# Optimization experiments

Hardware: AMD Instinct MI355X
Metric: run time of the kernel (lower is better)

Reference implementation:

```python
import jax, jax.numpy as jnp
import numpy as np

B, S, HID, HEADS = 1, 512, 1024, 16
HD = HID // HEADS          # 64
LN_EPS = 1e-5
EPS = 1e-8


def setup_inputs() -> dict:
    key = jax.random.key(0)
    ks = jax.random.split(key, 10)
    def w(k, fan_in, shape):
        return (jax.random.normal(k, shape, jnp.float32) / np.sqrt(fan_in)).astype(jnp.float32)
    return {
        "x": jax.random.normal(ks[0], (B, S, HID), jnp.float32),
        "attention_mask": jnp.ones((B, S), jnp.int32),
        "Wq": w(ks[1], HID, (HID, HID)), "bq": jnp.zeros((HID,), jnp.float32),
        "Wk": w(ks[2], HID, (HID, HID)), "bk": jnp.zeros((HID,), jnp.float32),
        "Wv": w(ks[3], HID, (HID, HID)), "bv": jnp.zeros((HID,), jnp.float32),
        "Wo": w(ks[4], HID, (HID, HID)), "bo": jnp.zeros((HID,), jnp.float32),
        "temperature": jnp.ones((1,), jnp.float32),
        "ln_gamma": jnp.ones((HID,), jnp.float32),
        "ln_beta": jnp.zeros((HID,), jnp.float32),
    }


def _forward(x, attention_mask, Wq, bq, Wk, bk, Wv, bv, Wo, bo, temperature, ln_gamma, ln_beta):
    b, s, hid = x.shape
    residual = x
    def proj(W, bias):  # [b,s,hid] -> [b,H,s,hd]
        return (x @ W + bias).reshape(b, s, HEADS, HD).transpose(0, 2, 1, 3)
    Q, K, V = proj(Wq, bq), proj(Wk, bk), proj(Wv, bv)
    # FFT over head_dim -> F = HD//2+1 frequency bins
    Qf = jnp.fft.rfft(Q, axis=-1)
    Kf = jnp.fft.rfft(K, axis=-1)
    Qa, Ka = jnp.abs(Qf), jnp.abs(Kf)
    Qp, Kp = jnp.angle(Qf), jnp.angle(Kf)
    # broadcast to [b,H,Sq,Sk,F]; eps lives inside sqrt (faithful, non-factorized)
    amp_w = jnp.sqrt(Qa[:, :, :, None, :] * Ka[:, :, None, :, :] + EPS)
    phase_align = jnp.cos(Qp[:, :, :, None, :] - Kp[:, :, None, :, :])
    scores = jnp.sum(phase_align * amp_w, axis=-1) * temperature  # [b,H,Sq,Sk]
    mask = attention_mask[:, None, None, :]  # [b,1,1,Sk]
    scores = jnp.where(mask == 0, jnp.float32(-1e9), scores)
    attn = jax.nn.softmax(scores, axis=-1)   # dropout omitted (eval mode)
    out = jnp.einsum('bhqk,bhkd->bhqd', attn, V)
    out = out.transpose(0, 2, 1, 3).reshape(b, s, hid)
    out = out @ Wo + bo
    y = residual + out
    mu = jnp.mean(y, axis=-1, keepdims=True)
    var = jnp.var(y, axis=-1, keepdims=True)
    return (y - mu) / jnp.sqrt(var + LN_EPS) * ln_gamma + ln_beta


def reference(x, attention_mask, Wq, bq, Wk, bk, Wv, bv, Wo, bo, temperature, ln_gamma, ln_beta):
    return _forward(x, attention_mask, Wq, bq, Wk, bk, Wv, bv, Wo, bo,
                    temperature, ln_gamma, ln_beta)
```

## Files before the change

kernel.cpp:

```cpp
#include <hip/hip_runtime.h>
#include <hip/hip_bf16.h>
#include <math.h>

constexpr int SEQ   = 512;
constexpr int HIDC  = 1024;
constexpr int NH    = 16;
constexpr int HDIM  = 64;
constexpr int NFREQ = 33;
constexpr int NFP   = 128;

typedef unsigned short u16;
typedef __bf16 bf16x8 __attribute__((ext_vector_type(8)));
typedef float  f32x4  __attribute__((ext_vector_type(4)));

typedef __attribute__((address_space(3))) void       as3_void;
typedef __attribute__((address_space(1))) const void as1_void;

__device__ __forceinline__ void gload16(const u16* g, u16* l) {
    __builtin_amdgcn_global_load_lds((as1_void*)g, (as3_void*)l, 16, 0, 0);
}

__device__ __forceinline__ float ldin(const void* p, int i, int f32) {
    if (f32) return ((const float*)p)[i];
    return __bfloat162float(((const __hip_bfloat16*)p)[i]);
}

__device__ __forceinline__ u16 f2b(float f) {
    unsigned int u = __builtin_bit_cast(unsigned int, f);
    u += 0x7fffu + ((u >> 16) & 1u);
    return (u16)(u >> 16);
}
__device__ __forceinline__ float b2f(u16 b) {
    return __builtin_bit_cast(float, (unsigned int)b << 16);
}
__device__ __forceinline__ void split2(float f, u16& hi, u16& lo) {
    hi = f2b(f);
    lo = f2b(f - b2f(hi));
}

__global__ void sniff_kernel(const void* w, int* flag) {
    __shared__ int cnt;
    if (threadIdx.x == 0) cnt = 0;
    __syncthreads();
    const unsigned short* h = (const unsigned short*)w;
    int bad = 0;
    for (int i = threadIdx.x; i < 512; i += 256) {
        const unsigned short v = h[i];
        const int ex = (v >> 7) & 0xFF;
        if (ex >= 134) bad++;
    }
    atomicAdd(&cnt, bad);
    __syncthreads();
    if (threadIdx.x == 0) flag[0] = (cnt > 32) ? 1 : 0;
}

__global__ __launch_bounds__(256) void prep_kernel(
    const void* __restrict__ W0, const void* __restrict__ W1,
    const void* __restrict__ W2, const void* __restrict__ W3,
    u16* __restrict__ H0, u16* __restrict__ L0,
    u16* __restrict__ H1, u16* __restrict__ L1,
    u16* __restrict__ H2, u16* __restrict__ L2,
    u16* __restrict__ H3, u16* __restrict__ L3,
    const void* __restrict__ xsrc, u16* __restrict__ xhi, u16* __restrict__ xlo,
    const int* __restrict__ flagp)
{
    const int F  = *flagp;
    const int mz = blockIdx.z;

    if (mz == 4) {
        const int blk = blockIdx.y * 16 + blockIdx.x;
        const int i0  = blk * 2048 + threadIdx.x * 8;
        #pragma unroll
        for (int g = 0; g < 2; ++g) {
            const int i = i0 + g * 4;
            float v[4];
            if (F) {
                const float4 f = *(const float4*)((const float*)xsrc + i);
                v[0] = f.x; v[1] = f.y; v[2] = f.z; v[3] = f.w;
            } else {
                #pragma unroll
                for (int j = 0; j < 4; ++j) v[j] = ldin(xsrc, i + j, 0);
            }
            ushort4 oh, ol;
            u16 h, l;
            split2(v[0], h, l); oh.x = h; ol.x = l;
            split2(v[1], h, l); oh.y = h; ol.y = l;
            split2(v[2], h, l); oh.z = h; ol.z = l;
            split2(v[3], h, l); oh.w = h; ol.w = l;
            *(ushort4*)&xhi[i] = oh;
            *(ushort4*)&xlo[i] = ol;
        }
        return;
    }

    __shared__ float t[64][65];
    const void* W = (mz == 0) ? W0 : (mz == 1) ? W1 : (mz == 2) ? W2 : W3;
    u16* H = (mz == 0) ? H0 : (mz == 1) ? H1 : (mz == 2) ? H2 : H3;
    u16* L = (mz == 0) ? L0 : (mz == 1) ? L1 : (mz == 2) ? L2 : L3;
    const int n0 = blockIdx.x * 64, k0 = blockIdx.y * 64;
    const int tid = threadIdx.x;

    #pragma unroll
    for (int i = 0; i < 4; ++i) {
        const int item = i * 256 + tid;
        const int r = item >> 4, c4 = (item & 15) * 4;
        if (F) {
            const float4 v = *(const float4*)((const float*)W + (k0 + r) * HIDC + n0 + c4);
            t[r][c4 + 0] = v.x; t[r][c4 + 1] = v.y; t[r][c4 + 2] = v.z; t[r][c4 + 3] = v.w;
        } else {
            #pragma unroll
            for (int j = 0; j < 4; ++j)
                t[r][c4 + j] = ldin(W, (k0 + r) * HIDC + n0 + c4 + j, 0);
        }
    }
    __syncthreads();
    #pragma unroll
    for (int i = 0; i < 4; ++i) {
        const int item = i * 256 + tid;
        const int r = item >> 4, c4 = (item & 15) * 4;
        ushort4 oh, ol;
        u16 h, l;
        split2(t[c4 + 0][r], h, l); oh.x = h; ol.x = l;
        split2(t[c4 + 1][r], h, l); oh.y = h; ol.y = l;
        split2(t[c4 + 2][r], h, l); oh.z = h; ol.z = l;
        split2(t[c4 + 3][r], h, l); oh.w = h; ol.w = l;
        *(ushort4*)&H[(n0 + r) * HIDC + k0 + c4] = oh;
        *(ushort4*)&L[(n0 + r) * HIDC + k0 + c4] = ol;
    }
}

template <int MODE>
__global__ __launch_bounds__(256) void mfma3_gemm_kernel(
    const u16* __restrict__ Ahi, const u16* __restrict__ Alo,
    const u16* __restrict__ B0h, const u16* __restrict__ B0l,
    const u16* __restrict__ B1h, const u16* __restrict__ B1l,
    const u16* __restrict__ B2h, const u16* __restrict__ B2l,
    const void* __restrict__ b0, const void* __restrict__ b1, const void* __restrict__ b2,
    const void* __restrict__ xres,
    float* __restrict__ O0, float* __restrict__ O1, float* __restrict__ O2,
    const int* __restrict__ flagp)
{
    __shared__ __align__(16) u16 smem[2 * 24576];
    const int F    = *flagp;
    const int tid  = threadIdx.x;
    const int lane = tid & 63, wv = tid >> 6;
    const int m0 = blockIdx.y * 64;
    const int n0 = blockIdx.x * 128;

    const u16 *Bh, *Bl; const void* bias; float* Out; int col0;
    if (MODE == 0) {
        const int mat = n0 >> 10;
        col0 = n0 & 1023;
        Bh   = (mat == 0) ? B0h : (mat == 1) ? B1h : B2h;
        Bl   = (mat == 0) ? B0l : (mat == 1) ? B1l : B2l;
        bias = (mat == 0) ? b0  : (mat == 1) ? b1  : b2;
        Out  = (mat == 0) ? O0  : (mat == 1) ? O1  : O2;
    } else {
        col0 = n0; Bh = B0h; Bl = B0l; bias = b0; Out = O0;
    }

    const int rsub = lane >> 3;
    const int gsw  = ((lane & 7) ^ rsub) * 8;
    const u16* pAh[2]; const u16* pAl[2];
    const u16* pBh[4]; const u16* pBl[4];
    int dA[2], dB[4];
    #pragma unroll
    for (int j = 0; j < 2; ++j) {
        const int c = wv * 2 + j;
        pAh[j] = Ahi + (m0 + c * 8 + rsub) * HIDC + gsw;
        pAl[j] = Alo + (m0 + c * 8 + rsub) * HIDC + gsw;
        dA[j]  = c * 512;
    }
    #pragma unroll
    for (int j = 0; j < 4; ++j) {
        const int c = wv * 4 + j;
        pBh[j] = Bh + (col0 + c * 8 + rsub) * HIDC + gsw;
        pBl[j] = Bl + (col0 + c * 8 + rsub) * HIDC + gsw;
        dB[j]  = c * 512;
    }

    int g16[2];
    #pragma unroll
    for (int kc = 0; kc < 2; ++kc) g16[kc] = (((kc * 4) + (lane >> 4)) ^ (lane & 7)) * 8;
    int afo[4], bfo[2];
    #pragma unroll
    for (int mi = 0; mi < 4; ++mi) afo[mi] = (mi * 16 + (lane & 15)) * 64;
    #pragma unroll
    for (int ni = 0; ni < 2; ++ni) bfo[ni] = (wv * 32 + ni * 16 + (lane & 15)) * 64;

    f32x4 zero = {0.f, 0.f, 0.f, 0.f};
    f32x4 acc[4][2];
    #pragma unroll
    for (int mi = 0; mi < 4; ++mi)
        #pragma unroll
        for (int ni = 0; ni < 2; ++ni) acc[mi][ni] = zero;

    #pragma unroll
    for (int j = 0; j < 2; ++j) {
        gload16(pAh[j], smem + dA[j]);
        gload16(pAl[j], smem + 4096 + dA[j]);
    }
    #pragma unroll
    for (int j = 0; j < 4; ++j) {
        gload16(pBh[j], smem + 8192  + dB[j]);
        gload16(pBl[j], smem + 16384 + dB[j]);
    }
    __syncthreads();

    for (int t = 0; t < 16; ++t) {
        const int bo = (t & 1) * 24576;
        if (t < 15) {
            const int bn = 24576 - bo;
            const int k  = (t + 1) * 64;
            #pragma unroll
            for (int j = 0; j < 2; ++j) {
                gload16(pAh[j] + k, smem + bn + dA[j]);
                gload16(pAl[j] + k, smem + bn + 4096 + dA[j]);
            }
            #pragma unroll
            for (int j = 0; j < 4; ++j) {
                gload16(pBh[j] + k, smem + bn + 8192  + dB[j]);
                gload16(pBl[j] + k, smem + bn + 16384 + dB[j]);
            }
        }
        #pragma unroll
        for (int kc = 0; kc < 2; ++kc) {
            bf16x8 ah[4], al[4], bh2[2], bl2[2];
            #pragma unroll
            for (int mi = 0; mi < 4; ++mi) {
                ah[mi] = *(const bf16x8*)(smem + bo +        afo[mi] + g16[kc]);
                al[mi] = *(const bf16x8*)(smem + bo + 4096 + afo[mi] + g16[kc]);
            }
            #pragma unroll
            for (int ni = 0; ni < 2; ++ni) {
                bh2[ni] = *(const bf16x8*)(smem + bo +  8192 + bfo[ni] + g16[kc]);
                bl2[ni] = *(const bf16x8*)(smem + bo + 16384 + bfo[ni] + g16[kc]);
            }
            #pragma unroll
            for (int mi = 0; mi < 4; ++mi)
                #pragma unroll
                for (int ni = 0; ni < 2; ++ni) {
                    acc[mi][ni] = __builtin_amdgcn_mfma_f32_16x16x32_bf16(
                        ah[mi], bh2[ni], acc[mi][ni], 0, 0, 0);
                    acc[mi][ni] = __builtin_amdgcn_mfma_f32_16x16x32_bf16(
                        ah[mi], bl2[ni], acc[mi][ni], 0, 0, 0);
                    acc[mi][ni] = __builtin_amdgcn_mfma_f32_16x16x32_bf16(
                        al[mi], bh2[ni], acc[mi][ni], 0, 0, 0);
                }
        }
        __syncthreads();
    }

    #pragma unroll
    for (int ni = 0; ni < 2; ++ni) {
        const int col = col0 + wv * 32 + ni * 16 + (lane & 15);
        const float bval = ldin(bias, col, F);
        #pragma unroll
        for (int mi = 0; mi < 4; ++mi) {
            const int row0 = m0 + mi * 16 + (lane >> 4) * 4;
            #pragma unroll
            for (int r = 0; r < 4; ++r) {
                const int row = row0 + r;
                float v = acc[mi][ni][r] + bval;
                if (MODE == 1) v += ldin(xres, row * HIDC + col, F);
                Out[row * HIDC + col] = v;
            }
        }
    }
}

__global__ __launch_bounds__(64) void spectral_kernel(
    const float* __restrict__ Q, const float* __restrict__ K,
    u16* __restrict__ Qsh, u16* __restrict__ Qsl,
    u16* __restrict__ Ksh, u16* __restrict__ Ksl)
{
    __shared__ float qv[64];
    __shared__ float tc[64], tsn[64];
    const int unit = blockIdx.x;
    const int sel  = blockIdx.y;
    const int s = unit >> 4, h = unit & 15;
    const float* src = sel ? K : Q;
    u16* dh = sel ? Ksh : Qsh;
    u16* dl = sel ? Ksl : Qsl;
    const int t = threadIdx.x;

    qv[t] = src[s * HIDC + h * HDIM + t];
    float sv, cv;
    sincosf((float)t * (6.283185307179586f / 64.0f), &sv, &cv);
    tc[t] = cv; tsn[t] = sv;
    __syncthreads();

    const int base = (h * SEQ + s) * NFP;
    if (t < NFREQ) {
        float re = 0.0f, im = 0.0f;
        #pragma unroll
        for (int k = 0; k < 64; ++k) {
            const int idx = (t * k) & 63;
            re = fmaf(qv[k], tc[idx], re);
            im = fmaf(qv[k], -tsn[idx], im);
        }
        const float a  = sqrtf(re * re + im * im);
        const float sc = (a > 0.0f) ? rsqrtf(a) : 0.0f;
        u16 hh, ll;
        split2(re * sc, hh, ll);
        dh[base + t] = hh; dl[base + t] = ll;
        split2(im * sc, hh, ll);
        dh[base + NFREQ + t] = hh; dl[base + NFREQ + t] = ll;
    }
    if (t < 62) {
        dh[base + 66 + t] = 0; dl[base + 66 + t] = 0;
    }
}

__global__ __launch_bounds__(256) void vtr_kernel(
    const float* __restrict__ V, u16* __restrict__ VTh, u16* __restrict__ VTl)
{
    __shared__ float t[64][65];
    const int s0 = blockIdx.x * 64, c0 = blockIdx.y * 64;
    const int tid = threadIdx.x;
    #pragma unroll
    for (int i = 0; i < 4; ++i) {
        const int item = i * 256 + tid;
        const int r = item >> 4, c4 = (item & 15) * 4;
        const float4 v = *(const float4*)&V[(s0 + r) * HIDC + c0 + c4];
        t[r][c4 + 0] = v.x; t[r][c4 + 1] = v.y; t[r][c4 + 2] = v.z; t[r][c4 + 3] = v.w;
    }
    __syncthreads();
    #pragma unroll
    for (int i = 0; i < 4; ++i) {
        const int item = i * 256 + tid;
        const int d = item >> 4, s4 = (item & 15) * 4;
        ushort4 oh, ol;
        u16 h, l;
        split2(t[s4 + 0][d], h, l); oh.x = h; ol.x = l;
        split2(t[s4 + 1][d], h, l); oh.y = h; ol.y = l;
        split2(t[s4 + 2][d], h, l); oh.z = h; ol.z = l;
        split2(t[s4 + 3][d], h, l); oh.w = h; ol.w = l;
        *(ushort4*)&VTh[(c0 + d) * SEQ + s0 + s4] = oh;
        *(ushort4*)&VTl[(c0 + d) * SEQ + s0 + s4] = ol;
    }
}

__global__ __launch_bounds__(128) void attn_mfma_kernel(
    const u16* __restrict__ Qsh, const u16* __restrict__ Qsl,
    const u16* __restrict__ Ksh, const u16* __restrict__ Ksl,
    const u16* __restrict__ VTh, const u16* __restrict__ VTl,
    const int* __restrict__ mask, const void* __restrict__ temp_p,
    u16* __restrict__ chi, u16* __restrict__ clo,
    const int* __restrict__ flagp)
{
    __shared__ __align__(16) u16 smem[32768];
    __shared__ int   mask_lds[512];
    __shared__ float mpart[2][16], lpart[2][16], l_final[16];

    const int F    = *flagp;
    const int tid  = threadIdx.x;
    const int lane = tid & 63, w = tid >> 6;
    const int hi = lane >> 4, q15 = lane & 15, l7 = lane & 7;
    const int h  = blockIdx.y, q0 = blockIdx.x * 16;
    const int k0 = w * 256;
    const int WB = w * 16384;
    const float temp = ldin(temp_p, 0, F);

    *(int4*)&mask_lds[tid * 4] = *(const int4*)&mask[tid * 4];

    bf16x8 qfh[3], qfl[3];
    {
        const int qrow = (h * SEQ + q0 + q15) * NFP;
        #pragma unroll
        for (int kc = 0; kc < 3; ++kc) {
            qfh[kc] = *(const bf16x8*)(Qsh + qrow + kc * 32 + hi * 8);
            qfl[kc] = *(const bf16x8*)(Qsl + qrow + kc * 32 + hi * 8);
        }
    }

    const int rc4 = lane >> 4;

    auto stageK = [&](int kt, int b) {
        const int base = WB + b * 8192;
        #pragma unroll
        for (int j = 0; j < 8; ++j) {
            const int row = j * 4 + rc4;
            const int gs  = (q15 ^ (row & 7)) * 8;
            const int so  = (h * SEQ + k0 + kt * 32 + row) * NFP + gs;
            gload16(Ksh + so, smem + base + j * 512);
            gload16(Ksl + so, smem + base + 4096 + j * 512);
        }
    };
    auto stageV = [&](int c, int b) {
        const int base = WB + b * 4096;
        #pragma unroll
        for (int j = 0; j < 4; ++j) {
            const int d  = j * 16 + (lane >> 2);
            const int gs = ((lane & 3) ^ (d & 3)) * 8;
            const int so = (h * HDIM + d) * SEQ + k0 + c * 32 + gs;
            gload16(VTh + so, smem + base + j * 512);
            gload16(VTl + so, smem + base + 2048 + j * 512);
        }
    };

    f32x4 sT[16];
    #pragma unroll
    for (int t = 0; t < 16; ++t) sT[t] = f32x4{0.f, 0.f, 0.f, 0.f};

    stageK(0, 0);
    #pragma unroll
    for (int kt = 0; kt < 8; ++kt) {
        if (kt < 7) {
            stageK(kt + 1, (kt + 1) & 1);
            asm volatile("s_waitcnt vmcnt(16)" ::: "memory");
        } else {
            asm volatile("s_waitcnt vmcnt(0)" ::: "memory");
        }
        __builtin_amdgcn_sched_barrier(0);
        const int base = WB + (kt & 1) * 8192;
        #pragma unroll
        for (int tt = 0; tt < 2; ++tt) {
            #pragma unroll
            for (int kc = 0; kc < 3; ++kc) {
                const int ro = (tt * 16 + q15) * 128 + (((kc * 4 + hi) ^ l7) * 8);
                const bf16x8 ah = *(const bf16x8*)(smem + base + ro);
                const bf16x8 al = *(const bf16x8*)(smem + base + 4096 + ro);
                sT[kt * 2 + tt] = __builtin_amdgcn_mfma_f32_16x16x32_bf16(ah, qfh[kc], sT[kt * 2 + tt], 0, 0, 0);
                sT[kt * 2 + tt] = __builtin_amdgcn_mfma_f32_16x16x32_bf16(ah, qfl[kc], sT[kt * 2 + tt], 0, 0, 0);
                sT[kt * 2 + tt] = __builtin_amdgcn_mfma_f32_16x16x32_bf16(al, qfh[kc], sT[kt * 2 + tt], 0, 0, 0);
            }
        }
    }

    __builtin_amdgcn_sched_barrier(0);
    stageV(0, 0);

    float m = -1e30f;
    #pragma unroll
    for (int t = 0; t < 16; ++t) {
        const int4 mv = *(const int4*)&mask_lds[k0 + t * 16 + hi * 4];
        float s;
        s = (mv.x == 0) ? -1e9f : sT[t][0] * temp; sT[t][0] = s; m = fmaxf(m, s);
        s = (mv.y == 0) ? -1e9f : sT[t][1] * temp; sT[t][1] = s; m = fmaxf(m, s);
        s = (mv.z == 0) ? -1e9f : sT[t][2] * temp; sT[t][2] = s; m = fmaxf(m, s);
        s = (mv.w == 0) ? -1e9f : sT[t][3] * temp; sT[t][3] = s; m = fmaxf(m, s);
    }
    m = fmaxf(m, __shfl_xor(m, 16, 64));
    m = fmaxf(m, __shfl_xor(m, 32, 64));
    if (lane < 16) mpart[w][q15] = m;
    __syncthreads();
    const float gm = fmaxf(mpart[0][q15], mpart[1][q15]);
    float sum = 0.0f;
    #pragma unroll
    for (int t = 0; t < 16; ++t) {
        #pragma unroll
        for (int r = 0; r < 4; ++r) {
            const float p = __expf(sT[t][r] - gm);
            sT[t][r] = p;
            sum += p;
        }
    }
    sum += __shfl_xor(sum, 16, 64);
    sum += __shfl_xor(sum, 32, 64);
    if (lane < 16) lpart[w][q15] = sum;
    __syncthreads();
    if (tid < 16) l_final[tid] = lpart[0][tid] + lpart[1][tid];

    const int PH = WB + 8192, PL = PH + 640;
    f32x4 acc[4];
    #pragma unroll
    for (int dt = 0; dt < 4; ++dt) acc[dt] = f32x4{0.f, 0.f, 0.f, 0.f};

    #pragma unroll
    for (int c = 0; c < 8; ++c) {
        if (c < 7) {
            stageV(c + 1, (c + 1) & 1);
            asm volatile("s_waitcnt vmcnt(8)" ::: "memory");
        } else {
            asm volatile("s_waitcnt vmcnt(0)" ::: "memory");
        }
        __builtin_amdgcn_sched_barrier(0);
        #pragma unroll
        for (int tt = 0; tt < 2; ++tt) {
            const int t = c * 2 + tt;
            ushort4 ph, pl;
            u16 hh, ll;
            split2(sT[t][0], hh, ll); ph.x = hh; pl.x = ll;
            split2(sT[t][1], hh, ll); ph.y = hh; pl.y = ll;
            split2(sT[t][2], hh, ll); ph.z = hh; pl.z = ll;
            split2(sT[t][3], hh, ll); ph.w = hh; pl.w = ll;
            const int g  = tt * 2 + (hi >> 1);
            const int po = q15 * 40 + ((g ^ (q15 & 3)) * 8) + (hi & 1) * 4;
            *(ushort4*)(smem + PH + po) = ph;
            *(ushort4*)(smem + PL + po) = pl;
        }
        const int vb  = WB + (c & 1) * 4096;
        const int pro = q15 * 40 + ((hi ^ (q15 & 3)) * 8);
        const bf16x8 pfh = *(const bf16x8*)(smem + PH + pro);
        const bf16x8 pfl = *(const bf16x8*)(smem + PL + pro);
        #pragma unroll
        for (int dt = 0; dt < 4; ++dt) {
            const int vo = (dt * 16 + q15) * 32 + ((hi ^ (q15 & 3)) * 8);
            const bf16x8 vfh = *(const bf16x8*)(smem + vb + vo);
            const bf16x8 vfl = *(const bf16x8*)(smem + vb + 2048 + vo);
            acc[dt] = __builtin_amdgcn_mfma_f32_16x16x32_bf16(pfh, vfh, acc[dt], 0, 0, 0);
            acc[dt] = __builtin_amdgcn_mfma_f32_16x16x32_bf16(pfl, vfh, acc[dt], 0, 0, 0);
            acc[dt] = __builtin_amdgcn_mfma_f32_16x16x32_bf16(pfh, vfl, acc[dt], 0, 0, 0);
        }
    }

    float* pacc = (float*)(smem + WB + 12288);
    #pragma unroll
    for (int dt = 0; dt < 4; ++dt)
        *(f32x4*)&pacc[(dt * 64 + lane) * 4] = acc[dt];
    __syncthreads();
    const float* pa0 = (const float*)(smem + 12288);
    const float* pa1 = (const float*)(smem + 16384 + 12288);
    #pragma unroll
    for (int dd = 0; dd < 2; ++dd) {
        const int dt = w * 2 + dd;
        #pragma unroll
        for (int r = 0; r < 4; ++r) {
            const int idx = (dt * 64 + lane) * 4 + r;
            const float v = (pa0[idx] + pa1[idx]) / l_final[hi * 4 + r];
            u16 hh, ll;
            split2(v, hh, ll);
            const int row = q0 + hi * 4 + r;
            const int col = h * HDIM + dt * 16 + q15;
            chi[row * HIDC + col] = hh;
            clo[row * HIDC + col] = ll;
        }
    }
}

__global__ __launch_bounds__(256) void ln_kernel(
    const float* __restrict__ Y, const void* __restrict__ gamma,
    const void* __restrict__ beta, void* __restrict__ out,
    const int* __restrict__ flagp)
{
    const int F = *flagp;
    const int row = blockIdx.x, tid = threadIdx.x;
    float v[4];
    float s = 0.0f, s2 = 0.0f;
    #pragma unroll
    for (int j = 0; j < 4; ++j) {
        v[j] = Y[row * HIDC + tid + j * 256];
        s += v[j]; s2 += v[j] * v[j];
    }
    #pragma unroll
    for (int off = 32; off > 0; off >>= 1) {
        s  += __shfl_xor(s, off, 64);
        s2 += __shfl_xor(s2, off, 64);
    }
    __shared__ float wred[4][2];
    const int w = tid >> 6;
    if ((tid & 63) == 0) { wred[w][0] = s; wred[w][1] = s2; }
    __syncthreads();
    s  = wred[0][0] + wred[1][0] + wred[2][0] + wred[3][0];
    s2 = wred[0][1] + wred[1][1] + wred[2][1] + wred[3][1];
    const float mu   = s / (float)HIDC;
    const float var  = s2 / (float)HIDC - mu * mu;
    const float rstd = rsqrtf(var + 1e-5f);
    #pragma unroll
    for (int j = 0; j < 4; ++j) {
        const int c = tid + j * 256;
        const float g = ldin(gamma, c, F), b = ldin(beta, c, F);
        const float r = (v[j] - mu) * rstd * g + b;
        if (F) ((float*)out)[row * HIDC + c] = r;
        else   ((__hip_bfloat16*)out)[row * HIDC + c] = __float2bfloat16(r);
    }
}

extern "C" void kernel_launch(void* const* d_in, const int* in_sizes, int n_in,
                              void* d_out, int out_size, void* d_ws, size_t ws_size,
                              hipStream_t stream) {
    const void* x    = d_in[0];
    const int*  mask = (const int*)d_in[1];
    const void* Wq   = d_in[2];
    const void* bq   = d_in[3];
    const void* Wk   = d_in[4];
    const void* bk   = d_in[5];
    const void* Wv   = d_in[6];
    const void* bv   = d_in[7];
    const void* Wo   = d_in[8];
    const void* bo   = d_in[9];
    const void* temp = d_in[10];
    const void* gam  = d_in[11];
    const void* bet  = d_in[12];

    float* ws   = (float*)d_ws;
    int*   flag = (int*)ws;
    float* Q    = ws + 4;
    float* K    = Q   + SEQ * HIDC;
    float* V    = K   + SEQ * HIDC;
    float* Y    = V   + SEQ * HIDC;
    u16*   xhi  = (u16*)(Y + SEQ * HIDC);
    u16*   xlo  = xhi + SEQ * HIDC;
    u16*   chi  = xlo + SEQ * HIDC;
    u16*   clo  = chi + SEQ * HIDC;
    u16*   Wqh  = clo + SEQ * HIDC;
    u16*   Wql  = Wqh + HIDC * HIDC;
    u16*   Wkh  = Wql + HIDC * HIDC;
    u16*   Wkl  = Wkh + HIDC * HIDC;
    u16*   Wvh  = Wkl + HIDC * HIDC;
    u16*   Wvl  = Wvh + HIDC * HIDC;
    u16*   Woh  = Wvl + HIDC * HIDC;
    u16*   Wol  = Woh + HIDC * HIDC;
    u16*   Qsh  = Wol + HIDC * HIDC;
    u16*   Qsl  = Qsh + NH * SEQ * NFP;
    u16*   Ksh  = Qsl + NH * SEQ * NFP;
    u16*   Ksl  = Ksh + NH * SEQ * NFP;
    u16*   VTh  = Ksl + NH * SEQ * NFP;
    u16*   VTl  = VTh + NH * HDIM * SEQ;

    sniff_kernel<<<1, 256, 0, stream>>>(Wq, flag);

    prep_kernel<<<dim3(16, 16, 5), 256, 0, stream>>>(
        Wq, Wk, Wv, Wo, Wqh, Wql, Wkh, Wkl, Wvh, Wvl, Woh, Wol,
        x, xhi, xlo, flag);

    mfma3_gemm_kernel<0><<<dim3(24, 8), 256, 0, stream>>>(
        xhi, xlo, Wqh, Wql, Wkh, Wkl, Wvh, Wvl,
        bq, bk, bv, nullptr, Q, K, V, flag);

    spectral_kernel<<<dim3(SEQ * NH, 2), 64, 0, stream>>>(Q, K, Qsh, Qsl, Ksh, Ksl);
    vtr_kernel<<<dim3(8, 16), 256, 0, stream>>>(V, VTh, VTl);

    attn_mfma_kernel<<<dim3(SEQ / 16, NH), 128, 0, stream>>>(
        Qsh, Qsl, Ksh, Ksl, VTh, VTl, mask, temp, chi, clo, flag);

    mfma3_gemm_kernel<1><<<dim3(8, 8), 256, 0, stream>>>(
        chi, clo, Woh, Wol, nullptr, nullptr, nullptr, nullptr,
        bo, nullptr, nullptr, x, Y, nullptr, nullptr, flag);

    ln_kernel<<<SEQ, 256, 0, stream>>>(Y, gam, bet, d_out, flag);
}
```

Baseline: 182.1 us.

## Fuse QKV epilogue into bf16 split, DFT via MFMA, inline dtype sniff

The QKV GEMM epilogue now writes hi/lo bf16 splits directly, and writes V already transposed, which removes the fp32 Q/K/V round trip and the separate transpose kernel. The per-token scalar spectral kernel becomes a batched DFT-as-GEMM kernel using MFMA against a cos/sin matrix built in registers. The standalone sniff kernel is removed and every kernel recomputes the dtype flag from a single wave read of Wq. The output projection moves to 32-row tiles so more blocks launch. This cuts launches and memory traffic, at the cost of redundant sniff loads and DFT rounding through split-bf16 MFMA.

New measurement: 161.6 us. 1.13x faster.

```diff
diff --git a/kernel.cpp b/kernel.cpp
--- a/kernel.cpp
+++ b/kernel.cpp
@@ -12,6 +12,7 @@
 typedef unsigned short u16;
 typedef __bf16 bf16x8 __attribute__((ext_vector_type(8)));
 typedef float  f32x4  __attribute__((ext_vector_type(4)));
+typedef unsigned short u16x8 __attribute__((ext_vector_type(8)));
 
 typedef __attribute__((address_space(3))) void       as3_void;
 typedef __attribute__((address_space(1))) const void as1_void;
@@ -38,20 +39,20 @@
     lo = f2b(f - b2f(hi));
 }
 
-__global__ void sniff_kernel(const void* w, int* flag) {
-    __shared__ int cnt;
-    if (threadIdx.x == 0) cnt = 0;
-    __syncthreads();
-    const unsigned short* h = (const unsigned short*)w;
+__device__ __forceinline__ int sniffF(const u16* wq) {
+    const int lane = threadIdx.x & 63;
+    const ushort4 a = *(const ushort4*)(wq + lane * 8);
+    const ushort4 b = *(const ushort4*)(wq + lane * 8 + 4);
     int bad = 0;
-    for (int i = threadIdx.x; i < 512; i += 256) {
-        const unsigned short v = h[i];
-        const int ex = (v >> 7) & 0xFF;
-        if (ex >= 134) bad++;
-    }
-    atomicAdd(&cnt, bad);
-    __syncthreads();
-    if (threadIdx.x == 0) flag[0] = (cnt > 32) ? 1 : 0;
+    {
+        const u16 vs[8] = {a.x, a.y, a.z, a.w, b.x, b.y, b.z, b.w};
+        #pragma unroll
+        for (int j = 0; j < 8; ++j)
+            if (((vs[j] >> 7) & 0xFF) >= 134) bad++;
+    }
+    #pragma unroll
+    for (int off = 32; off > 0; off >>= 1) bad += __shfl_xor(bad, off, 64);
+    return (bad > 32) ? 1 : 0;
 }
 
 __global__ __launch_bounds__(256) void prep_kernel(
@@ -61,10 +62,9 @@
     u16* __restrict__ H1, u16* __restrict__ L1,
     u16* __restrict__ H2, u16* __restrict__ L2,
     u16* __restrict__ H3, u16* __restrict__ L3,
-    const void* __restrict__ xsrc, u16* __restrict__ xhi, u16* __restrict__ xlo,
-    const int* __restrict__ flagp)
+    const void* __restrict__ xsrc, u16* __restrict__ xhi, u16* __restrict__ xlo)
 {
-    const int F  = *flagp;
+    const int F  = sniffF((const u16*)W0);
     const int mz = blockIdx.z;
 
     if (mz == 4) {
@@ -129,7 +129,7 @@
     }
 }
 
-template <int MODE>
+template <int MODE, int MT>
 __global__ __launch_bounds__(256) void mfma3_gemm_kernel(
     const u16* __restrict__ Ahi, const u16* __restrict__ Alo,
     const u16* __restrict__ B0h, const u16* __restrict__ B0l,
@@ -137,26 +137,33 @@
     const u16* __restrict__ B2h, const u16* __restrict__ B2l,
     const void* __restrict__ b0, const void* __restrict__ b1, const void* __restrict__ b2,
     const void* __restrict__ xres,
-    float* __restrict__ O0, float* __restrict__ O1, float* __restrict__ O2,
-    const int* __restrict__ flagp)
+    u16* __restrict__ Qh, u16* __restrict__ Ql,
+    u16* __restrict__ Kh, u16* __restrict__ Kl,
+    u16* __restrict__ Vth, u16* __restrict__ Vtl,
+    float* __restrict__ Yout,
+    const void* __restrict__ wq_sniff)
 {
-    __shared__ __align__(16) u16 smem[2 * 24576];
-    const int F    = *flagp;
+    constexpr int NMI = MT / 16;
+    constexpr int NAC = MT / 32;
+    constexpr int ACH = MT * 64;
+    constexpr int BUF = 2 * ACH + 16384;
+    __shared__ __align__(16) u16 smem[2 * BUF];
+
+    const int F    = sniffF((const u16*)wq_sniff);
     const int tid  = threadIdx.x;
     const int lane = tid & 63, wv = tid >> 6;
-    const int m0 = blockIdx.y * 64;
+    const int m0 = blockIdx.y * MT;
     const int n0 = blockIdx.x * 128;
 
-    const u16 *Bh, *Bl; const void* bias; float* Out; int col0;
+    const u16 *Bh, *Bl; const void* bias; int col0, mat = 0;
     if (MODE == 0) {
-        const int mat = n0 >> 10;
+        mat  = n0 >> 10;
         col0 = n0 & 1023;
         Bh   = (mat == 0) ? B0h : (mat == 1) ? B1h : B2h;
         Bl   = (mat == 0) ? B0l : (mat == 1) ? B1l : B2l;
         bias = (mat == 0) ? b0  : (mat == 1) ? b1  : b2;
-        Out  = (mat == 0) ? O0  : (mat == 1) ? O1  : O2;
     } else {
-        col0 = n0; Bh = B0h; Bl = B0l; bias = b0; Out = O0;
+        col0 = n0; Bh = B0h; Bl = B0l; bias = b0;
     }
 
     const int rsub = lane >> 3;
@@ -165,8 +172,8 @@
     const u16* pBh[4]; const u16* pBl[4];
     int dA[2], dB[4];
     #pragma unroll
-    for (int j = 0; j < 2; ++j) {
-        const int c = wv * 2 + j;
+    for (int j = 0; j < NAC; ++j) {
+        const int c = wv * NAC + j;
         pAh[j] = Ahi + (m0 + c * 8 + rsub) * HIDC + gsw;
         pAl[j] = Alo + (m0 + c * 8 + rsub) * HIDC + gsw;
         dA[j]  = c * 512;
@@ -184,60 +191,59 @@
     for (int kc = 0; kc < 2; ++kc) g16[kc] = (((kc * 4) + (lane >> 4)) ^ (lane & 7)) * 8;
     int afo[4], bfo[2];
     #pragma unroll
-    for (int mi = 0; mi < 4; ++mi) afo[mi] = (mi * 16 + (lane & 15)) * 64;
+    for (int mi = 0; mi < NMI; ++mi) afo[mi] = (mi * 16 + (lane & 15)) * 64;
     #pragma unroll
     for (int ni = 0; ni < 2; ++ni) bfo[ni] = (wv * 32 + ni * 16 + (lane & 15)) * 64;
 
-    f32x4 zero = {0.f, 0.f, 0.f, 0.f};
-    f32x4 acc[4][2];
-    #pragma unroll
-    for (int mi = 0; mi < 4; ++mi)
-        #pragma unroll
-        for (int ni = 0; ni < 2; ++ni) acc[mi][ni] = zero;
-
-    #pragma unroll
-    for (int j = 0; j < 2; ++j) {
+    f32x4 acc[NMI][2];
+    #pragma unroll
+    for (int mi = 0; mi < NMI; ++mi)
+        #pragma unroll
+        for (int ni = 0; ni < 2; ++ni) acc[mi][ni] = f32x4{0.f, 0.f, 0.f, 0.f};
+
+    #pragma unroll
+    for (int j = 0; j < NAC; ++j) {
         gload16(pAh[j], smem + dA[j]);
-        gload16(pAl[j], smem + 4096 + dA[j]);
+        gload16(pAl[j], smem + ACH + dA[j]);
     }
     #pragma unroll
     for (int j = 0; j < 4; ++j) {
-        gload16(pBh[j], smem + 8192  + dB[j]);
-        gload16(pBl[j], smem + 16384 + dB[j]);
+        gload16(pBh[j], smem + 2 * ACH + dB[j]);
+        gload16(pBl[j], smem + 2 * ACH + 8192 + dB[j]);
     }
     __syncthreads();
 
     for (int t = 0; t < 16; ++t) {
-        const int bo = (t & 1) * 24576;
+        const int bo = (t & 1) * BUF;
         if (t < 15) {
-            const int bn = 24576 - bo;
+            const int bn = BUF - bo;
             const int k  = (t + 1) * 64;
             #pragma unroll
-            for (int j = 0; j < 2; ++j) {
+            for (int j = 0; j < NAC; ++j) {
                 gload16(pAh[j] + k, smem + bn + dA[j]);
-                gload16(pAl[j] + k, smem + bn + 4096 + dA[j]);
+                gload16(pAl[j] + k, smem + bn + ACH + dA[j]);
             }
             #pragma unroll
             for (int j = 0; j < 4; ++j) {
-                gload16(pBh[j] + k, smem + bn + 8192  + dB[j]);
-                gload16(pBl[j] + k, smem + bn + 16384 + dB[j]);
+                gload16(pBh[j] + k, smem + bn + 2 * ACH + dB[j]);
+                gload16(pBl[j] + k, smem + bn + 2 * ACH + 8192 + dB[j]);
             }
         }
         #pragma unroll
         for (int kc = 0; kc < 2; ++kc) {
-            bf16x8 ah[4], al[4], bh2[2], bl2[2];
-            #pragma unroll
-            for (int mi = 0; mi < 4; ++mi) {
-                ah[mi] = *(const bf16x8*)(smem + bo +        afo[mi] + g16[kc]);
-                al[mi] = *(const bf16x8*)(smem + bo + 4096 + afo[mi] + g16[kc]);
+            bf16x8 ah[NMI], al[NMI], bh2[2], bl2[2];
+            #pragma unroll
+            for (int mi = 0; mi < NMI; ++mi) {
+                ah[mi] = *(const bf16x8*)(smem + bo +       afo[mi] + g16[kc]);
+                al[mi] = *(const bf16x8*)(smem + bo + ACH + afo[mi] + g16[kc]);
             }
             #pragma unroll
             for (int ni = 0; ni < 2; ++ni) {
-                bh2[ni] = *(const bf16x8*)(smem + bo +  8192 + bfo[ni] + g16[kc]);
-                bl2[ni] = *(const bf16x8*)(smem + bo + 16384 + bfo[ni] + g16[kc]);
-            }
-            #pragma unroll
-            for (int mi = 0; mi < 4; ++mi)
+                bh2[ni] = *(const bf16x8*)(smem + bo + 2 * ACH +        bfo[ni] + g16[kc]);
+                bl2[ni] = *(const bf16x8*)(smem + bo + 2 * ACH + 8192 + bfo[ni] + g16[kc]);
+            }
+            #pragma unroll
+            for (int mi = 0; mi < NMI; ++mi)
                 #pragma unroll
                 for (int ni = 0; ni < 2; ++ni) {
                     acc[mi][ni] = __builtin_amdgcn_mfma_f32_16x16x32_bf16(
@@ -251,93 +257,167 @@
         __syncthreads();
     }
 
+    const int hi4 = (lane >> 4) * 4;
     #pragma unroll
     for (int ni = 0; ni < 2; ++ni) {
         const int col = col0 + wv * 32 + ni * 16 + (lane & 15);
         const float bval = ldin(bias, col, F);
         #pragma unroll
-        for (int mi = 0; mi < 4; ++mi) {
-            const int row0 = m0 + mi * 16 + (lane >> 4) * 4;
-            #pragma unroll
-            for (int r = 0; r < 4; ++r) {
-                const int row = row0 + r;
-                float v = acc[mi][ni][r] + bval;
-                if (MODE == 1) v += ldin(xres, row * HIDC + col, F);
-                Out[row * HIDC + col] = v;
-            }
-        }
-    }
-}
-
-__global__ __launch_bounds__(64) void spectral_kernel(
-    const float* __restrict__ Q, const float* __restrict__ K,
+        for (int mi = 0; mi < NMI; ++mi) {
+            const int row0 = m0 + mi * 16 + hi4;
+            if (MODE == 1) {
+                #pragma unroll
+                for (int r = 0; r < 4; ++r) {
+                    const int row = row0 + r;
+                    Yout[row * HIDC + col] =
+                        acc[mi][ni][r] + bval + ldin(xres, row * HIDC + col, F);
+                }
+            } else if (mat == 2) {
+                ushort4 oh, ol;
+                u16 h_, l_;
+                split2(acc[mi][ni][0] + bval, h_, l_); oh.x = h_; ol.x = l_;
+                split2(acc[mi][ni][1] + bval, h_, l_); oh.y = h_; ol.y = l_;
+                split2(acc[mi][ni][2] + bval, h_, l_); oh.z = h_; ol.z = l_;
+                split2(acc[mi][ni][3] + bval, h_, l_); oh.w = h_; ol.w = l_;
+                *(ushort4*)&Vth[col * SEQ + row0] = oh;
+                *(ushort4*)&Vtl[col * SEQ + row0] = ol;
+            } else {
+                u16* Oh = (mat == 0) ? Qh : Kh;
+                u16* Ol = (mat == 0) ? Ql : Kl;
+                #pragma unroll
+                for (int r = 0; r < 4; ++r) {
+                    u16 h_, l_;
+                    split2(acc[mi][ni][r] + bval, h_, l_);
+                    Oh[(row0 + r) * HIDC + col] = h_;
+                    Ol[(row0 + r) * HIDC + col] = l_;
+                }
+            }
+        }
+    }
+}
+
+__global__ __launch_bounds__(256) void dft_kernel(
+    const u16* __restrict__ Qmh, const u16* __restrict__ Qml,
+    const u16* __restrict__ Kmh, const u16* __restrict__ Kml,
     u16* __restrict__ Qsh, u16* __restrict__ Qsl,
     u16* __restrict__ Ksh, u16* __restrict__ Ksl)
 {
-    __shared__ float qv[64];
-    __shared__ float tc[64], tsn[64];
-    const int unit = blockIdx.x;
-    const int sel  = blockIdx.y;
-    const int s = unit >> 4, h = unit & 15;
-    const float* src = sel ? K : Q;
-    u16* dh = sel ? Ksh : Qsh;
-    u16* dl = sel ? Ksl : Qsl;
-    const int t = threadIdx.x;
-
-    qv[t] = src[s * HIDC + h * HDIM + t];
-    float sv, cv;
-    sincosf((float)t * (6.283185307179586f / 64.0f), &sv, &cv);
-    tc[t] = cv; tsn[t] = sv;
-    __syncthreads();
-
-    const int base = (h * SEQ + s) * NFP;
-    if (t < NFREQ) {
-        float re = 0.0f, im = 0.0f;
-        #pragma unroll
-        for (int k = 0; k < 64; ++k) {
-            const int idx = (t * k) & 63;
-            re = fmaf(qv[k], tc[idx], re);
-            im = fmaf(qv[k], -tsn[idx], im);
-        }
-        const float a  = sqrtf(re * re + im * im);
-        const float sc = (a > 0.0f) ? rsqrtf(a) : 0.0f;
-        u16 hh, ll;
-        split2(re * sc, hh, ll);
-        dh[base + t] = hh; dl[base + t] = ll;
-        split2(im * sc, hh, ll);
-        dh[base + NFREQ + t] = hh; dl[base + NFREQ + t] = ll;
-    }
-    if (t < 62) {
-        dh[base + 66 + t] = 0; dl[base + 66 + t] = 0;
-    }
-}
-
-__global__ __launch_bounds__(256) void vtr_kernel(
-    const float* __restrict__ V, u16* __restrict__ VTh, u16* __restrict__ VTl)
-{
-    __shared__ float t[64][65];
-    const int s0 = blockIdx.x * 64, c0 = blockIdx.y * 64;
-    const int tid = threadIdx.x;
-    #pragma unroll
-    for (int i = 0; i < 4; ++i) {
-        const int item = i * 256 + tid;
-        const int r = item >> 4, c4 = (item & 15) * 4;
-        const float4 v = *(const float4*)&V[(s0 + r) * HIDC + c0 + c4];
-        t[r][c4 + 0] = v.x; t[r][c4 + 1] = v.y; t[r][c4 + 2] = v.z; t[r][c4 + 3] = v.w;
-    }
-    __syncthreads();
-    #pragma unroll
-    for (int i = 0; i < 4; ++i) {
-        const int item = i * 256 + tid;
-        const int d = item >> 4, s4 = (item & 15) * 4;
+    __shared__ __align__(16) u16 smem[16384];
+    __shared__ float tcos[64], tsin[64];
+
+    const int tid  = threadIdx.x;
+    const int lane = tid & 63, wv = tid >> 6;
+    const int hi = lane >> 4, q15 = lane & 15, l7 = lane & 7;
+    const int m0  = blockIdx.x * 64;
+    const int sel = blockIdx.y;
+    const u16* Ah_g = sel ? Kmh : Qmh;
+    const u16* Al_g = sel ? Kml : Qml;
+    u16* Oh = sel ? Ksh : Qsh;
+    u16* Ol = sel ? Ksl : Qsl;
+
+    const int rsub = lane >> 3;
+    const int gsw  = ((lane & 7) ^ rsub) * 8;
+    #pragma unroll
+    for (int j = 0; j < 2; ++j) {
+        const int c = wv * 2 + j;
+        gload16(Ah_g + (m0 + c * 8 + rsub) * 64 + gsw, smem + c * 512);
+        gload16(Al_g + (m0 + c * 8 + rsub) * 64 + gsw, smem + 4096 + c * 512);
+    }
+    if (tid < 64) {
+        float sv, cv;
+        sincosf((float)tid * (6.283185307179586f / 64.0f), &sv, &cv);
+        tcos[tid] = cv; tsin[tid] = sv;
+    }
+    __syncthreads();
+
+    bf16x8 Dh[2][2], Dl[2][2];
+    #pragma unroll
+    for (int ni = 0; ni < 2; ++ni) {
+        const int c = wv * 32 + ni * 16 + q15;
+        #pragma unroll
+        for (int kc = 0; kc < 2; ++kc) {
+            u16x8 bh_, bl_;
+            #pragma unroll
+            for (int e = 0; e < 8; ++e) {
+                const int k = (kc * 4 + hi) * 8 + e;
+                float dv;
+                if (c < 33)      dv = tcos[(c * k) & 63];
+                else if (c < 66) dv = -tsin[((c - 33) * k) & 63];
+                else             dv = 0.0f;
+                u16 h_, l_;
+                split2(dv, h_, l_);
+                bh_[e] = h_; bl_[e] = l_;
+            }
+            Dh[ni][kc] = __builtin_bit_cast(bf16x8, bh_);
+            Dl[ni][kc] = __builtin_bit_cast(bf16x8, bl_);
+        }
+    }
+
+    f32x4 acc[4][2];
+    #pragma unroll
+    for (int mi = 0; mi < 4; ++mi)
+        #pragma unroll
+        for (int ni = 0; ni < 2; ++ni) acc[mi][ni] = f32x4{0.f, 0.f, 0.f, 0.f};
+
+    #pragma unroll
+    for (int kc = 0; kc < 2; ++kc) {
+        const int g = (((kc * 4) + hi) ^ l7) * 8;
+        bf16x8 ah[4], al[4];
+        #pragma unroll
+        for (int mi = 0; mi < 4; ++mi) {
+            ah[mi] = *(const bf16x8*)(smem +        (mi * 16 + q15) * 64 + g);
+            al[mi] = *(const bf16x8*)(smem + 4096 + (mi * 16 + q15) * 64 + g);
+        }
+        #pragma unroll
+        for (int mi = 0; mi < 4; ++mi)
+            #pragma unroll
+            for (int ni = 0; ni < 2; ++ni) {
+                acc[mi][ni] = __builtin_amdgcn_mfma_f32_16x16x32_bf16(
+                    ah[mi], Dh[ni][kc], acc[mi][ni], 0, 0, 0);
+                acc[mi][ni] = __builtin_amdgcn_mfma_f32_16x16x32_bf16(
+                    ah[mi], Dl[ni][kc], acc[mi][ni], 0, 0, 0);
+                acc[mi][ni] = __builtin_amdgcn_mfma_f32_16x16x32_bf16(
+                    al[mi], Dh[ni][kc], acc[mi][ni], 0, 0, 0);
+            }
+    }
+    __syncthreads();
+
+    float* Cl = (float*)smem;
+    #pragma unroll
+    for (int mi = 0; mi < 4; ++mi)
+        #pragma unroll
+        for (int ni = 0; ni < 2; ++ni)
+            #pragma unroll
+            for (int r = 0; r < 4; ++r)
+                Cl[(mi * 16 + hi * 4 + r) * 128 + wv * 32 + ni * 16 + q15] = acc[mi][ni][r];
+    __syncthreads();
+
+    const int row = tid >> 2, tf = tid & 3;
+    const int g   = m0 + row;
+    const int ss  = g >> 4, hh = g & 15;
+    u16 vh[32], vl[32];
+    #pragma unroll
+    for (int j = 0; j < 32; ++j) {
+        const int f = tf * 32 + j;
+        float val = 0.0f;
+        if (f < 66) {
+            const int fb = (f < 33) ? f : (f - 33);
+            const float re = Cl[row * 128 + fb];
+            const float im = Cl[row * 128 + 33 + fb];
+            const float a  = sqrtf(re * re + im * im);
+            const float sc = (a > 0.0f) ? rsqrtf(a) : 0.0f;
+            val = ((f < 33) ? re : im) * sc;
+        }
+        split2(val, vh[j], vl[j]);
+    }
+    const int obase = (hh * SEQ + ss) * NFP + tf * 32;
+    #pragma unroll
+    for (int j4 = 0; j4 < 8; ++j4) {
         ushort4 oh, ol;
-        u16 h, l;
-        split2(t[s4 + 0][d], h, l); oh.x = h; ol.x = l;
-        split2(t[s4 + 1][d], h, l); oh.y = h; ol.y = l;
-        split2(t[s4 + 2][d], h, l); oh.z = h; ol.z = l;
-        split2(t[s4 + 3][d], h, l); oh.w = h; ol.w = l;
-        *(ushort4*)&VTh[(c0 + d) * SEQ + s0 + s4] = oh;
-        *(ushort4*)&VTl[(c0 + d) * SEQ + s0 + s4] = ol;
+        oh.x = vh[j4 * 4 + 0]; oh.y = vh[j4 * 4 + 1]; oh.z = vh[j4 * 4 + 2]; oh.w = vh[j4 * 4 + 3];
+        ol.x = vl[j4 * 4 + 0]; ol.y = vl[j4 * 4 + 1]; ol.z = vl[j4 * 4 + 2]; ol.w = vl[j4 * 4 + 3];
+        *(ushort4*)&Oh[obase + j4 * 4] = oh;
+        *(ushort4*)&Ol[obase + j4 * 4] = ol;
     }
 }
 
@@ -347,13 +427,13 @@
     const u16* __restrict__ VTh, const u16* __restrict__ VTl,
     const int* __restrict__ mask, const void* __restrict__ temp_p,
     u16* __restrict__ chi, u16* __restrict__ clo,
-    const int* __restrict__ flagp)
+    const void* __restrict__ wq_sniff)
 {
     __shared__ __align__(16) u16 smem[32768];
     __shared__ int   mask_lds[512];
     __shared__ float mpart[2][16], lpart[2][16], l_final[16];
 
-    const int F    = *flagp;
+    const int F    = sniffF((const u16*)wq_sniff);
     const int tid  = threadIdx.x;
     const int lane = tid & 63, w = tid >> 6;
     const int hi = lane >> 4, q15 = lane & 15, l7 = lane & 7;
@@ -532,9 +612,9 @@
 __global__ __launch_bounds__(256) void ln_kernel(
     const float* __restrict__ Y, const void* __restrict__ gamma,
     const void* __restrict__ beta, void* __restrict__ out,
-    const int* __restrict__ flagp)
+    const void* __restrict__ wq_sniff)
 {
-    const int F = *flagp;
+    const int F = sniffF((const u16*)wq_sniff);
     const int row = blockIdx.x, tid = threadIdx.x;
     float v[4];
     float s = 0.0f, s2 = 0.0f;
@@ -584,17 +664,18 @@
     const void* gam  = d_in[11];
     const void* bet  = d_in[12];
 
-    float* ws   = (float*)d_ws;
-    int*   flag = (int*)ws;
-    float* Q    = ws + 4;
-    float* K    = Q   + SEQ * HIDC;
-    float* V    = K   + SEQ * HIDC;
-    float* Y    = V   + SEQ * HIDC;
+    float* Y    = (float*)d_ws;
     u16*   xhi  = (u16*)(Y + SEQ * HIDC);
     u16*   xlo  = xhi + SEQ * HIDC;
     u16*   chi  = xlo + SEQ * HIDC;
     u16*   clo  = chi + SEQ * HIDC;
-    u16*   Wqh  = clo + SEQ * HIDC;
+    u16*   Qmh  = clo + SEQ * HIDC;
+    u16*   Qml  = Qmh + SEQ * HIDC;
+    u16*   Kmh  = Qml + SEQ * HIDC;
+    u16*   Kml  = Kmh + SEQ * HIDC;
+    u16*   VTh  = Kml + SEQ * HIDC;
+    u16*   VTl  = VTh + NH * HDIM * SEQ;
+    u16*   Wqh  = VTl + NH * HDIM * SEQ;
     u16*   Wql  = Wqh + HIDC * HIDC;
     u16*   Wkh  = Wql + HIDC * HIDC;
     u16*   Wkl  = Wkh + HIDC * HIDC;
@@ -606,28 +687,26 @@
     u16*   Qsl  = Qsh + NH * SEQ * NFP;
     u16*   Ksh  = Qsl + NH * SEQ * NFP;
     u16*   Ksl  = Ksh + NH * SEQ * NFP;
-    u16*   VTh  = Ksl + NH * SEQ * NFP;
-    u16*   VTl  = VTh + NH * HDIM * SEQ;
-
-    sniff_kernel<<<1, 256, 0, stream>>>(Wq, flag);
 
     prep_kernel<<<dim3(16, 16, 5), 256, 0, stream>>>(
         Wq, Wk, Wv, Wo, Wqh, Wql, Wkh, Wkl, Wvh, Wvl, Woh, Wol,
-        x, xhi, xlo, flag);
-
-    mfma3_gemm_kernel<0><<<dim3(24, 8), 256, 0, stream>>>(
+        x, xhi, xlo);
+
+    mfma3_gemm_kernel<0, 64><<<dim3(24, 8), 256, 0, stream>>>(
         xhi, xlo, Wqh, Wql, Wkh, Wkl, Wvh, Wvl,
-        bq, bk, bv, nullptr, Q, K, V, flag);
-
-    spectral_kernel<<<dim3(SEQ * NH, 2), 64, 0, stream>>>(Q, K, Qsh, Qsl, Ksh, Ksl);
-    vtr_kernel<<<dim3(8, 16), 256, 0, stream>>>(V, VTh, VTl);
+        bq, bk, bv, nullptr,
+        Qmh, Qml, Kmh, Kml, VTh, VTl, nullptr, Wq);
+
+    dft_kernel<<<dim3(128, 2), 256, 0, stream>>>(
+        Qmh, Qml, Kmh, Kml, Qsh, Qsl, Ksh, Ksl);
 
     attn_mfma_kernel<<<dim3(SEQ / 16, NH), 128, 0, stream>>>(
-        Qsh, Qsl, Ksh, Ksl, VTh, VTl, mask, temp, chi, clo, flag);
-
-    mfma3_gemm_kernel<1><<<dim3(8, 8), 256, 0, stream>>>(
+        Qsh, Qsl, Ksh, Ksl, VTh, VTl, mask, temp, chi, clo, Wq);
+
+    mfma3_gemm_kernel<1, 32><<<dim3(8, 16), 256, 0, stream>>>(
         chi, clo, Woh, Wol, nullptr, nullptr, nullptr, nullptr,
-        bo, nullptr, nullptr, x, Y, nullptr, nullptr, flag);
-
-    ln_kernel<<<SEQ, 256, 0, stream>>>(Y, gam, bet, d_out, flag);
-}
+        bo, nullptr, nullptr, x,
+        nullptr, nullptr, nullptr, nullptr, nullptr, nullptr, Y, Wq);
+
+    ln_kernel<<<SEQ, 256, 0, stream>>>(Y, gam, bet, d_out, Wq);
+}
```
